# Optimization experiments

Measured on AMD Instinct MI355X. Metric: run time of the kernel, lower is better.

Reference implementation:

```python
import jax, jax.numpy as jnp
import numpy as np

HEADS = 16


def setup_inputs() -> dict:
    key = jax.random.key(0)
    k1, k2, k3, k4 = jax.random.split(key, 4)
    B, S, D = 2, 2048, 1024
    x = jax.random.normal(k1, (B, S, D), dtype=jnp.float32)
    scale = 0.02
    Wq = jax.random.normal(k2, (D, D), dtype=jnp.float32) * scale
    Wk = jax.random.normal(k3, (D, D), dtype=jnp.float32) * scale
    Wv = jax.random.normal(k4, (D, D), dtype=jnp.float32) * scale
    return {"x": x, "Wq": Wq, "Wk": Wk, "Wv": Wv}


def reference(x, Wq, Wk, Wv):
    B, S, D = x.shape
    H = HEADS
    dh = D // H
    # project and split heads: (B, S, D) -> (B, H, S, dh)
    def split_heads(t):
        return t.reshape(B, S, H, dh).transpose(0, 2, 1, 3)

    q = split_heads(x @ Wq)
    k = split_heads(x @ Wk)
    v = split_heads(x @ Wv)

    # scores: (B, H, S, S)
    scores = jnp.einsum("bhqd,bhkd->bhqk", q, k)
    causal_mask = jnp.triu(jnp.ones((S, S), dtype=bool), k=1)  # True above diagonal -> masked
    scores = jnp.where(causal_mask, -jnp.inf, scores) / jnp.sqrt(jnp.float32(dh))
    weights = jax.nn.softmax(scores, axis=-1)
    # dropout is identity at inference (eval mode)
    ctx = jnp.einsum("bhqk,bhkd->bhqd", weights, v)  # (B, H, S, dh)
    return ctx.transpose(0, 2, 1, 3).reshape(B, S, D)
```

## Files before the change

kernel.cpp:

```cpp
#include <hip/hip_runtime.h>
#include <hip/hip_bf16.h>
#include <cstdint>

#define BATCH  2
#define SEQ    2048
#define DMODEL 1024
#define NH     16
#define DH     64

typedef short bf16x8 __attribute__((ext_vector_type(8)));
typedef float f32x4  __attribute__((ext_vector_type(4)));
typedef unsigned short u16;

#define MFMA16(a, b, c) __builtin_amdgcn_mfma_f32_16x16x32_bf16((a), (b), (c), 0, 0, 0)

#define GLL(gp, lp) __builtin_amdgcn_global_load_lds( \
    (const __attribute__((address_space(1))) void*)(gp), \
    (__attribute__((address_space(3))) void*)(lp), 16, 0, 0)

#define SCL 0.18033688011112042f

#if __has_builtin(__builtin_amdgcn_exp2f)
#define EXP2(x) __builtin_amdgcn_exp2f(x)
#else
#define EXP2(x) __expf((x) * 0.69314718055994531f)
#endif

static __device__ __forceinline__ u16 f2bf(float f) {
  union { float f; unsigned int i; } u; u.f = f;
  unsigned int r = u.i + 0x7FFFu + ((u.i >> 16) & 1u);
  return (u16)(r >> 16);
}

__global__ __launch_bounds__(256) void convert_x_kernel(const float* __restrict__ X,
                                                        u16* __restrict__ Xb) {
  int idx = (blockIdx.x * 256 + threadIdx.x) * 8;
  float4 a = *reinterpret_cast<const float4*>(X + idx);
  float4 b = *reinterpret_cast<const float4*>(X + idx + 4);
  union { bf16x8 v; u16 u[8]; } pk;
  pk.u[0]=f2bf(a.x); pk.u[1]=f2bf(a.y); pk.u[2]=f2bf(a.z); pk.u[3]=f2bf(a.w);
  pk.u[4]=f2bf(b.x); pk.u[5]=f2bf(b.y); pk.u[6]=f2bf(b.z); pk.u[7]=f2bf(b.w);
  *reinterpret_cast<bf16x8*>(Xb + idx) = pk.v;
}

__global__ __launch_bounds__(256) void transpose_w_kernel(const float* __restrict__ W0,
                                                          const float* __restrict__ W1,
                                                          const float* __restrict__ W2,
                                                          u16* __restrict__ Wt) {
  const float* W = (blockIdx.z == 0) ? W0 : (blockIdx.z == 1) ? W1 : W2;
  const float sc = (blockIdx.z == 0) ? SCL : 1.0f;
  u16* out = Wt + (size_t)blockIdx.z * DMODEL * DMODEL;
  __shared__ float T[32][33];
  const int t = threadIdx.x;
  const int k0 = blockIdx.x * 32, n0 = blockIdx.y * 32;
  {
    int r = t >> 3, c = (t & 7) * 4;
    float4 v = *reinterpret_cast<const float4*>(W + (size_t)(k0 + r) * DMODEL + n0 + c);
    T[r][c] = v.x; T[r][c+1] = v.y; T[r][c+2] = v.z; T[r][c+3] = v.w;
  }
  __syncthreads();
  {
    int n = t >> 3, k = (t & 7) * 4;
    union { unsigned long long ll; u16 u[4]; } pk;
    pk.u[0] = f2bf(T[k][n] * sc);   pk.u[1] = f2bf(T[k+1][n] * sc);
    pk.u[2] = f2bf(T[k+2][n] * sc); pk.u[3] = f2bf(T[k+3][n] * sc);
    *reinterpret_cast<unsigned long long*>(out + (size_t)(n0 + n) * DMODEL + k0 + k) = pk.ll;
  }
}

__global__ __launch_bounds__(256) void qkv_mfma_kernel(const u16* __restrict__ Xb,
                                                       const u16* __restrict__ Wt,
                                                       u16* __restrict__ Y) {
  __shared__ u16 As[128 * 64];
  __shared__ u16 Bs[128 * 64];
  char* Ab = (char*)As; char* Bb = (char*)Bs;
  const int t = threadIdx.x;
  const int lane = t & 63;
  const int w = t >> 6;
  const int wr = w >> 1, wc = w & 1;
  const int l15 = lane & 15, lg = lane >> 4;
  const int row0 = blockIdx.x * 128;
  const int col0 = blockIdx.y * 128;
  const int z = blockIdx.z;
  const u16* Wz = Wt + (size_t)z * DMODEL * DMODEL;
  u16* Yz = Y + (size_t)z * ((size_t)BATCH * SEQ * DMODEL);

  f32x4 acc[4][4];
  #pragma unroll
  for (int mt = 0; mt < 4; ++mt)
    #pragma unroll
    for (int nt = 0; nt < 4; ++nt)
      acc[mt][nt] = (f32x4){0.f, 0.f, 0.f, 0.f};

  size_t aofs[4], bofs[4];
  #pragma unroll
  for (int it = 0; it < 4; ++it) {
    int row = it * 32 + (t >> 3);
    int sl  = (t & 7) ^ (row & 7);
    aofs[it] = (size_t)(row0 + row) * DMODEL + sl * 8;
    bofs[it] = (size_t)(col0 + row) * DMODEL + sl * 8;
  }

  for (int k0 = 0; k0 < DMODEL; k0 += 64) {
    __syncthreads();
    #pragma unroll
    for (int it = 0; it < 4; ++it) {
      GLL(Xb + aofs[it] + k0, Ab + it * 4096 + w * 1024);
      GLL(Wz + bofs[it] + k0, Bb + it * 4096 + w * 1024);
    }
    __syncthreads();
    #pragma unroll
    for (int c = 0; c < 2; ++c) {
      bf16x8 am[4], bn[4];
      int kof = c * 64 + lg * 16;
      #pragma unroll
      for (int mt = 0; mt < 4; ++mt) {
        int row = wr * 64 + mt * 16 + l15;
        am[mt] = *reinterpret_cast<const bf16x8*>(Ab + row * 128 + (kof ^ ((row & 7) << 4)));
      }
      #pragma unroll
      for (int nt = 0; nt < 4; ++nt) {
        int row = wc * 64 + nt * 16 + l15;
        bn[nt] = *reinterpret_cast<const bf16x8*>(Bb + row * 128 + (kof ^ ((row & 7) << 4)));
      }
      #pragma unroll
      for (int mt = 0; mt < 4; ++mt)
        #pragma unroll
        for (int nt = 0; nt < 4; ++nt)
          acc[mt][nt] = MFMA16(am[mt], bn[nt], acc[mt][nt]);
    }
  }

  #pragma unroll
  for (int mt = 0; mt < 4; ++mt) {
    #pragma unroll
    for (int i = 0; i < 4; ++i) {
      int bs = row0 + wr * 64 + mt * 16 + lg * 4 + i;
      int b = bs >> 11, s = bs & (SEQ - 1);
      #pragma unroll
      for (int nt = 0; nt < 4; ++nt) {
        int d = col0 + wc * 64 + nt * 16 + l15;
        int h = d >> 6, dd = d & (DH - 1);
        size_t off = (((size_t)b * NH + h) * SEQ + s) * DH + dd;
        Yz[off] = f2bf(acc[mt][nt][i]);
      }
    }
  }
}

__global__ __launch_bounds__(256) void transpose_v_kernel(const u16* __restrict__ V,
                                                          u16* __restrict__ Vt) {
  __shared__ u16 L[64][72];
  const int sb = blockIdx.x, h = blockIdx.y, b = blockIdx.z;
  const size_t hin  = ((size_t)b * NH + h) * (size_t)SEQ * DH;
  const size_t hout = ((size_t)b * NH + h) * (size_t)DH * SEQ;
  const int s0 = sb * 64;
  const int t = threadIdx.x;
  const int r = t >> 3, c = t & 7;
  #pragma unroll
  for (int it = 0; it < 2; ++it) {
    int row = r + it * 32;
    bf16x8 v = *reinterpret_cast<const bf16x8*>(V + hin + (size_t)(s0 + row) * DH + c * 8);
    *reinterpret_cast<bf16x8*>(&L[row][c * 8]) = v;
  }
  __syncthreads();
  #pragma unroll
  for (int it = 0; it < 2; ++it) {
    int d = r + it * 32;
    union { bf16x8 v; u16 u[8]; } pk;
    #pragma unroll
    for (int j = 0; j < 8; ++j) pk.u[j] = L[c * 8 + j][d];
    *reinterpret_cast<bf16x8*>(Vt + hout + (size_t)d * SEQ + s0 + c * 8) = pk.v;
  }
}

#define STAGE(kb)                                                     \
  {                                                                   \
    const u16* kp_ = Kw + hq + (size_t)(kb) * (64 * DH);              \
    const u16* vp_ = Vt + hv + (size_t)(kb) * 64;                     \
    _Pragma("unroll")                                                 \
    for (int it = 0; it < 8; ++it) {                                  \
      GLL(kp_ + kofs[it], (char*)Ksb + it * 1024);                    \
      GLL(vp_ + vofs[it], (char*)Vsb + it * 1024);                    \
    }                                                                 \
  }

#define WAITV()                                                       \
  asm volatile("s_waitcnt vmcnt(0)" ::: "memory");                    \
  __builtin_amdgcn_sched_barrier(0)

#define TILE(kbv, MASKED)                                                            \
  {                                                                                  \
    char* Kb = (char*)Ksb;                                                           \
    char* Vb = (char*)Vsb;                                                           \
    const int k0_ = (kbv) * 64;                                                      \
    __builtin_amdgcn_s_setprio(1);                                                   \
    _Pragma("unroll")                                                                \
    for (int kt = 0; kt < 4; ++kt) {                                                 \
      bf16x8 kf0 = *reinterpret_cast<const bf16x8*>(Kb + kvb0 + kt * 2048);          \
      bf16x8 kf1 = *reinterpret_cast<const bf16x8*>(Kb + kvb1 + kt * 2048);          \
      f32x4 sA = (f32x4){0.f, 0.f, 0.f, 0.f};                                        \
      f32x4 sB = (f32x4){0.f, 0.f, 0.f, 0.f};                                        \
      sA = MFMA16(kf0, qfA0, sA); sA = MFMA16(kf1, qfA1, sA);                        \
      sB = MFMA16(kf0, qfB0, sB); sB = MFMA16(kf1, qfB1, sB);                        \
      union { unsigned long long ll; __hip_bfloat16 bf[4]; } pA, pB;                 \
      _Pragma("unroll")                                                              \
      for (int i = 0; i < 4; ++i) {                                                  \
        float svA = sA[i], svB = sB[i];                                              \
        if (MASKED) {                                                                \
          int key = k0_ + kt * 16 + lg * 4 + i;                                      \
          if (key > qrowA) svA = -1e30f;                                             \
          if (key > qrowB) svB = -1e30f;                                             \
        }                                                                            \
        float eA = EXP2(svA), eB = EXP2(svB);                                        \
        l_A += eA; l_B += eB;                                                        \
        pA.bf[i] = __float2bfloat16(eA);                                             \
        pB.bf[i] = __float2bfloat16(eB);                                             \
      }                                                                              \
      int kx = (kt * 32) ^ xw;                                                       \
      *reinterpret_cast<unsigned long long*>(PbW + pwA + kx) = pA.ll;                \
      *reinterpret_cast<unsigned long long*>(PbW + pwB + kx) = pB.ll;                \
    }                                                                                \
    _Pragma("unroll")                                                                \
    for (int kc = 0; kc < 2; ++kc) {                                                 \
      const int tg = kc * 64;                                                        \
      bf16x8 paA = *reinterpret_cast<const bf16x8*>(PbW + (kvb0 ^ tg));              \
      bf16x8 paB = *reinterpret_cast<const bf16x8*>(PbW + (kvb0 ^ tg) + 2048);       \
      _Pragma("unroll")                                                              \
      for (int dt = 0; dt < 4; ++dt) {                                               \
        bf16x8 vv = *reinterpret_cast<const bf16x8*>(Vb + (kvb0 ^ tg) + dt * 2048);  \
        oA[dt] = MFMA16(paA, vv, oA[dt]);                                            \
        oB[dt] = MFMA16(paB, vv, oB[dt]);                                            \
      }                                                                              \
    }                                                                                \
    __builtin_amdgcn_s_setprio(0);                                                   \
  }

__global__ __launch_bounds__(64) void flash_mfma10_kernel(const u16* __restrict__ Qw,
                                                          const u16* __restrict__ Kw,
                                                          const u16* __restrict__ Vt,
                                                          float* __restrict__ Out) {
  __shared__ u16 Ksb[64 * 64];
  __shared__ u16 Vsb[64 * 64];
  __shared__ u16 Pw[32 * 64];

  const int wgid = blockIdx.x;
  const int g = wgid & 31;
  const int j = (wgid >> 5) & 7;
  const int r = wgid >> 8;
  const int qt = r * 8 + ((r & 1) ? (7 - j) : j);
  const int b = g >> 4, h = g & 15;
  const int nkv = (qt >> 1) + 1;

  const int lane = threadIdx.x;
  const int l15 = lane & 15, lg = lane >> 4;
  char* PbW = (char*)Pw;
  const size_t hq = ((size_t)b * NH + h) * (size_t)SEQ * DH;
  const size_t hv = ((size_t)b * NH + h) * (size_t)DH * SEQ;

  int kofs[8], vofs[8];
  #pragma unroll
  for (int it = 0; it < 8; ++it) {
    int idx = it * 64 + lane;
    int row = idx >> 3, sl = idx & 7;
    kofs[it] = row * DH  + ((sl ^ (row & 7)) * 8);
    vofs[it] = row * SEQ + ((sl ^ (row & 7)) * 8);
  }

  const int kvb0 = l15 * 128 + ((lg * 16) ^ ((l15 & 3) << 4)) + ((l15 & 4) << 4);
  const int kvb1 = kvb0 ^ 64;
  const int pwA  = l15 * 128 + ((lg * 8) ^ ((l15 & 1) << 4));
  const int pwB  = pwA + 2048;
  const int xw   = ((l15 >> 1) & 3) << 5;

  const int qbase = qt * 32;
  const int qrowA = qbase + l15;
  const int qrowB = qbase + 16 + l15;

  bf16x8 qfA0, qfA1, qfB0, qfB1;
  {
    const u16* qpA = Qw + hq + (size_t)qrowA * DH + lg * 8;
    const u16* qpB = Qw + hq + (size_t)qrowB * DH + lg * 8;
    qfA0 = *reinterpret_cast<const bf16x8*>(qpA);
    qfA1 = *reinterpret_cast<const bf16x8*>(qpA + 32);
    qfB0 = *reinterpret_cast<const bf16x8*>(qpB);
    qfB1 = *reinterpret_cast<const bf16x8*>(qpB + 32);
  }

  f32x4 oA[4], oB[4];
  #pragma unroll
  for (int dt = 0; dt < 4; ++dt) {
    oA[dt] = (f32x4){0.f, 0.f, 0.f, 0.f};
    oB[dt] = (f32x4){0.f, 0.f, 0.f, 0.f};
  }
  float l_A = 0.f, l_B = 0.f;

  #pragma unroll 1
  for (int kb = 0; kb < nkv - 1; ++kb) {
    STAGE(kb);
    WAITV();
    TILE(kb, 0);
  }
  STAGE(nkv - 1);
  WAITV();
  TILE(nkv - 1, 1);

  l_A += __shfl_xor(l_A, 16); l_A += __shfl_xor(l_A, 32);
  l_B += __shfl_xor(l_B, 16); l_B += __shfl_xor(l_B, 32);
  #pragma unroll
  for (int i = 0; i < 4; ++i) {
    float liA = __shfl(l_A, (lane & 48) + lg * 4 + i);
    float liB = __shfl(l_B, (lane & 48) + lg * 4 + i);
    float invA = 1.f / liA, invB = 1.f / liB;
    int qA = qbase + lg * 4 + i;
    int qB = qbase + 16 + lg * 4 + i;
    float* opA = Out + ((size_t)b * SEQ + qA) * DMODEL + h * DH + l15;
    float* opB = Out + ((size_t)b * SEQ + qB) * DMODEL + h * DH + l15;
    #pragma unroll
    for (int dt = 0; dt < 4; ++dt) {
      opA[dt * 16] = oA[dt][i] * invA;
      opB[dt * 16] = oB[dt][i] * invB;
    }
  }
}

extern "C" void kernel_launch(void* const* d_in, const int* in_sizes, int n_in,
                              void* d_out, int out_size, void* d_ws, size_t ws_size,
                              hipStream_t stream) {
  const float* x  = (const float*)d_in[0];
  const float* Wq = (const float*)d_in[1];
  const float* Wk = (const float*)d_in[2];
  const float* Wv = (const float*)d_in[3];
  float* out = (float*)d_out;

  u16* ws  = (u16*)d_ws;
  u16* qkv = ws;
  u16* xb  = ws + 12582912;
  u16* wt  = ws + 16777216;
  u16* vt  = ws + 19922944;

  convert_x_kernel<<<2048, 256, 0, stream>>>(x, xb);
  transpose_w_kernel<<<dim3(32, 32, 3), 256, 0, stream>>>(Wq, Wk, Wv, wt);
  qkv_mfma_kernel<<<dim3(32, 8, 3), 256, 0, stream>>>(xb, wt, qkv);
  transpose_v_kernel<<<dim3(32, NH, BATCH), 256, 0, stream>>>(qkv + 8388608, vt);
  flash_mfma10_kernel<<<2048, 64, 0, stream>>>(qkv, qkv + 4194304, vt, out);
}
```

Baseline: 99.11 us.

## Double-buffer K/V tiles in flash kernel and schedule longest query tiles first

Adds a second LDS buffer for K and V so the next tile's global-to-LDS loads are issued before computing the current tile. Partial vmcnt waits let those loads overlap the MFMA work. Workgroups are also reordered so the query tiles with the most KV blocks launch first, which is meant to reduce tail imbalance under the causal mask. LDS per single-wave workgroup grows from about 20KB to 36KB, which may reduce how many workgroups fit on a CU.

After: 93.35 us. 5.8% less time.

```diff
diff --git a/kernel.cpp b/kernel.cpp
--- a/kernel.cpp
+++ b/kernel.cpp
@@ -174,25 +174,25 @@
   }
 }
 
-#define STAGE(kb)                                                     \
+#define STAGE(KD, VD, kb)                                             \
   {                                                                   \
     const u16* kp_ = Kw + hq + (size_t)(kb) * (64 * DH);              \
     const u16* vp_ = Vt + hv + (size_t)(kb) * 64;                     \
     _Pragma("unroll")                                                 \
     for (int it = 0; it < 8; ++it) {                                  \
-      GLL(kp_ + kofs[it], (char*)Ksb + it * 1024);                    \
-      GLL(vp_ + vofs[it], (char*)Vsb + it * 1024);                    \
+      GLL(kp_ + kofs[it], (char*)(KD) + it * 1024);                   \
+      GLL(vp_ + vofs[it], (char*)(VD) + it * 1024);                   \
     }                                                                 \
   }
 
-#define WAITV()                                                       \
-  asm volatile("s_waitcnt vmcnt(0)" ::: "memory");                    \
+#define WAITC(N)                                                      \
+  asm volatile("s_waitcnt vmcnt(" #N ")" ::: "memory");               \
   __builtin_amdgcn_sched_barrier(0)
 
-#define TILE(kbv, MASKED)                                                            \
+#define TILE(kbv, KBUF, VBUF, MASKED)                                                \
   {                                                                                  \
-    char* Kb = (char*)Ksb;                                                           \
-    char* Vb = (char*)Vsb;                                                           \
+    char* Kb = (char*)(KBUF);                                                        \
+    char* Vb = (char*)(VBUF);                                                        \
     const int k0_ = (kbv) * 64;                                                      \
     __builtin_amdgcn_s_setprio(1);                                                   \
     _Pragma("unroll")                                                                \
@@ -236,19 +236,19 @@
     __builtin_amdgcn_s_setprio(0);                                                   \
   }
 
-__global__ __launch_bounds__(64) void flash_mfma10_kernel(const u16* __restrict__ Qw,
+__global__ __launch_bounds__(64) void flash_mfma11_kernel(const u16* __restrict__ Qw,
                                                           const u16* __restrict__ Kw,
                                                           const u16* __restrict__ Vt,
                                                           float* __restrict__ Out) {
-  __shared__ u16 Ksb[64 * 64];
-  __shared__ u16 Vsb[64 * 64];
+  __shared__ u16 KsA[64 * 64];
+  __shared__ u16 KsB[64 * 64];
+  __shared__ u16 VsA[64 * 64];
+  __shared__ u16 VsB[64 * 64];
   __shared__ u16 Pw[32 * 64];
 
   const int wgid = blockIdx.x;
   const int g = wgid & 31;
-  const int j = (wgid >> 5) & 7;
-  const int r = wgid >> 8;
-  const int qt = r * 8 + ((r & 1) ? (7 - j) : j);
+  const int qt = 63 - (wgid >> 5);
   const int b = g >> 4, h = g & 15;
   const int nkv = (qt >> 1) + 1;
 
@@ -295,15 +295,28 @@
   }
   float l_A = 0.f, l_B = 0.f;
 
+  STAGE(KsA, VsA, 0);
+  int kb = 0;
   #pragma unroll 1
-  for (int kb = 0; kb < nkv - 1; ++kb) {
-    STAGE(kb);
-    WAITV();
-    TILE(kb, 0);
-  }
-  STAGE(nkv - 1);
-  WAITV();
-  TILE(nkv - 1, 1);
+  while (kb + 2 < nkv) {
+    STAGE(KsB, VsB, kb + 1);
+    WAITC(16);
+    TILE(kb, KsA, VsA, 0);
+    STAGE(KsA, VsA, kb + 2);
+    WAITC(16);
+    TILE(kb + 1, KsB, VsB, 0);
+    kb += 2;
+  }
+  if (kb + 2 == nkv) {
+    STAGE(KsB, VsB, kb + 1);
+    WAITC(16);
+    TILE(kb, KsA, VsA, 0);
+    WAITC(0);
+    TILE(kb + 1, KsB, VsB, 1);
+  } else {
+    WAITC(0);
+    TILE(kb, KsA, VsA, 1);
+  }
 
   l_A += __shfl_xor(l_A, 16); l_A += __shfl_xor(l_A, 32);
   l_B += __shfl_xor(l_B, 16); l_B += __shfl_xor(l_B, 32);
@@ -343,5 +356,5 @@
   transpose_w_kernel<<<dim3(32, 32, 3), 256, 0, stream>>>(Wq, Wk, Wv, wt);
   qkv_mfma_kernel<<<dim3(32, 8, 3), 256, 0, stream>>>(xb, wt, qkv);
   transpose_v_kernel<<<dim3(32, NH, BATCH), 256, 0, stream>>>(qkv + 8388608, vt);
-  flash_mfma10_kernel<<<2048, 64, 0, stream>>>(qkv, qkv + 4194304, vt, out);
-}
+  flash_mfma11_kernel<<<2048, 64, 0, stream>>>(qkv, qkv + 4194304, vt, out);
+}
```

## Split long causal rows across two workgroups and read K/V directly from global

Applied to the files above, without the earlier changes.

Query tiles in the upper half are split into two KV-range partitions, each written as an unnormalized bf16 partial with row sums, and a new reduce kernel combines them. The aim is to balance causal work across workgroups and shorten the tail, using 3072 workgroups instead of 2048. The LDS staging of K and V through global_load_lds is also removed, so MFMA operands are read straight from global memory. This cuts LDS use and barriers but depends on cache hits, and it adds an extra launch plus bf16 rounding of the partial outputs. Combining without a max is valid because the kernel never subtracts a running max.

Result: slower. 126.8 us (+27.9%).

```diff
diff --git a/kernel.cpp b/kernel.cpp
--- a/kernel.cpp
+++ b/kernel.cpp
@@ -30,6 +30,11 @@
   union { float f; unsigned int i; } u; u.f = f;
   unsigned int r = u.i + 0x7FFFu + ((u.i >> 16) & 1u);
   return (u16)(r >> 16);
+}
+
+static __device__ __forceinline__ float bf2f(u16 v) {
+  union { unsigned int i; float f; } u; u.i = ((unsigned int)v) << 16;
+  return u.f;
 }
 
 __global__ __launch_bounds__(256) void convert_x_kernel(const float* __restrict__ X,
@@ -174,83 +179,73 @@
   }
 }
 
-#define STAGE(kb)                                                     \
-  {                                                                   \
-    const u16* kp_ = Kw + hq + (size_t)(kb) * (64 * DH);              \
-    const u16* vp_ = Vt + hv + (size_t)(kb) * 64;                     \
-    _Pragma("unroll")                                                 \
-    for (int it = 0; it < 8; ++it) {                                  \
-      GLL(kp_ + kofs[it], (char*)Ksb + it * 1024);                    \
-      GLL(vp_ + vofs[it], (char*)Vsb + it * 1024);                    \
-    }                                                                 \
-  }
-
-#define WAITV()                                                       \
-  asm volatile("s_waitcnt vmcnt(0)" ::: "memory");                    \
-  __builtin_amdgcn_sched_barrier(0)
-
-#define TILE(kbv, MASKED)                                                            \
-  {                                                                                  \
-    char* Kb = (char*)Ksb;                                                           \
-    char* Vb = (char*)Vsb;                                                           \
-    const int k0_ = (kbv) * 64;                                                      \
-    __builtin_amdgcn_s_setprio(1);                                                   \
-    _Pragma("unroll")                                                                \
-    for (int kt = 0; kt < 4; ++kt) {                                                 \
-      bf16x8 kf0 = *reinterpret_cast<const bf16x8*>(Kb + kvb0 + kt * 2048);          \
-      bf16x8 kf1 = *reinterpret_cast<const bf16x8*>(Kb + kvb1 + kt * 2048);          \
-      f32x4 sA = (f32x4){0.f, 0.f, 0.f, 0.f};                                        \
-      f32x4 sB = (f32x4){0.f, 0.f, 0.f, 0.f};                                        \
-      sA = MFMA16(kf0, qfA0, sA); sA = MFMA16(kf1, qfA1, sA);                        \
-      sB = MFMA16(kf0, qfB0, sB); sB = MFMA16(kf1, qfB1, sB);                        \
-      union { unsigned long long ll; __hip_bfloat16 bf[4]; } pA, pB;                 \
-      _Pragma("unroll")                                                              \
-      for (int i = 0; i < 4; ++i) {                                                  \
-        float svA = sA[i], svB = sB[i];                                              \
-        if (MASKED) {                                                                \
-          int key = k0_ + kt * 16 + lg * 4 + i;                                      \
-          if (key > qrowA) svA = -1e30f;                                             \
-          if (key > qrowB) svB = -1e30f;                                             \
-        }                                                                            \
-        float eA = EXP2(svA), eB = EXP2(svB);                                        \
-        l_A += eA; l_B += eB;                                                        \
-        pA.bf[i] = __float2bfloat16(eA);                                             \
-        pB.bf[i] = __float2bfloat16(eB);                                             \
-      }                                                                              \
-      int kx = (kt * 32) ^ xw;                                                       \
-      *reinterpret_cast<unsigned long long*>(PbW + pwA + kx) = pA.ll;                \
-      *reinterpret_cast<unsigned long long*>(PbW + pwB + kx) = pB.ll;                \
-    }                                                                                \
-    _Pragma("unroll")                                                                \
-    for (int kc = 0; kc < 2; ++kc) {                                                 \
-      const int tg = kc * 64;                                                        \
-      bf16x8 paA = *reinterpret_cast<const bf16x8*>(PbW + (kvb0 ^ tg));              \
-      bf16x8 paB = *reinterpret_cast<const bf16x8*>(PbW + (kvb0 ^ tg) + 2048);       \
-      _Pragma("unroll")                                                              \
-      for (int dt = 0; dt < 4; ++dt) {                                               \
-        bf16x8 vv = *reinterpret_cast<const bf16x8*>(Vb + (kvb0 ^ tg) + dt * 2048);  \
-        oA[dt] = MFMA16(paA, vv, oA[dt]);                                            \
-        oB[dt] = MFMA16(paB, vv, oB[dt]);                                            \
-      }                                                                              \
-    }                                                                                \
-    __builtin_amdgcn_s_setprio(0);                                                   \
-  }
-
-__global__ __launch_bounds__(64) void flash_mfma10_kernel(const u16* __restrict__ Qw,
-                                                          const u16* __restrict__ Kw,
-                                                          const u16* __restrict__ Vt,
-                                                          float* __restrict__ Out) {
-  __shared__ u16 Ksb[64 * 64];
-  __shared__ u16 Vsb[64 * 64];
+#define TILE(kbv, MASKED)                                                             \
+  {                                                                                   \
+    const int k0_ = (kbv) * 64;                                                       \
+    const u16* kp_ = Kw + hq + (size_t)k0_ * DH;                                      \
+    const u16* vp_ = Vt + hv + k0_;                                                   \
+    __builtin_amdgcn_s_setprio(1);                                                    \
+    _Pragma("unroll")                                                                 \
+    for (int kt = 0; kt < 4; ++kt) {                                                  \
+      const u16* kr_ = kp_ + (kt * 16 + l15) * DH + lg * 8;                           \
+      bf16x8 kf0 = *reinterpret_cast<const bf16x8*>(kr_);                             \
+      bf16x8 kf1 = *reinterpret_cast<const bf16x8*>(kr_ + 32);                        \
+      f32x4 sA = (f32x4){0.f, 0.f, 0.f, 0.f};                                         \
+      f32x4 sB = (f32x4){0.f, 0.f, 0.f, 0.f};                                         \
+      sA = MFMA16(kf0, qfA0, sA); sA = MFMA16(kf1, qfA1, sA);                         \
+      sB = MFMA16(kf0, qfB0, sB); sB = MFMA16(kf1, qfB1, sB);                         \
+      union { unsigned long long ll; __hip_bfloat16 bf[4]; } pA, pB;                  \
+      _Pragma("unroll")                                                               \
+      for (int i = 0; i < 4; ++i) {                                                   \
+        float svA = sA[i], svB = sB[i];                                               \
+        if (MASKED) {                                                                 \
+          int key = k0_ + kt * 16 + lg * 4 + i;                                       \
+          if (key > qrowA) svA = -1e30f;                                              \
+          if (key > qrowB) svB = -1e30f;                                              \
+        }                                                                             \
+        float eA = EXP2(svA), eB = EXP2(svB);                                         \
+        l_A += eA; l_B += eB;                                                         \
+        pA.bf[i] = __float2bfloat16(eA);                                              \
+        pB.bf[i] = __float2bfloat16(eB);                                              \
+      }                                                                               \
+      int kx = (kt * 32) ^ xw;                                                        \
+      *reinterpret_cast<unsigned long long*>(PbW + pwA + kx) = pA.ll;                 \
+      *reinterpret_cast<unsigned long long*>(PbW + pwB + kx) = pB.ll;                 \
+    }                                                                                 \
+    _Pragma("unroll")                                                                 \
+    for (int kc = 0; kc < 2; ++kc) {                                                  \
+      const int tg = kc * 64;                                                         \
+      bf16x8 paA = *reinterpret_cast<const bf16x8*>(PbW + (kvb0 ^ tg));               \
+      bf16x8 paB = *reinterpret_cast<const bf16x8*>(PbW + (kvb0 ^ tg) + 2048);        \
+      _Pragma("unroll")                                                               \
+      for (int dt = 0; dt < 4; ++dt) {                                                \
+        bf16x8 vv = *reinterpret_cast<const bf16x8*>(vp_ + (size_t)(dt * 16 + l15) * SEQ + kc * 32 + lg * 8); \
+        oA[dt] = MFMA16(paA, vv, oA[dt]);                                             \
+        oB[dt] = MFMA16(paB, vv, oB[dt]);                                             \
+      }                                                                               \
+    }                                                                                 \
+    __builtin_amdgcn_s_setprio(0);                                                    \
+  }
+
+__global__ __launch_bounds__(64) void flash_part_kernel(const u16* __restrict__ Qw,
+                                                        const u16* __restrict__ Kw,
+                                                        const u16* __restrict__ Vt,
+                                                        u16* __restrict__ Pws,
+                                                        float* __restrict__ Out) {
   __shared__ u16 Pw[32 * 64];
 
   const int wgid = blockIdx.x;
+  const int up = wgid >> 5;
   const int g = wgid & 31;
-  const int j = (wgid >> 5) & 7;
-  const int r = wgid >> 8;
-  const int qt = r * 8 + ((r & 1) ? (7 - j) : j);
+  int qt, c;
+  if (up < 32)      { qt = 32 + up;   c = 0; }
+  else if (up < 64) { qt = 63 - up;   c = 0; }
+  else              { qt = 127 - up;  c = 1; }
   const int b = g >> 4, h = g & 15;
   const int nkv = (qt >> 1) + 1;
+  const int kbeg = c * 16;
+  const int kend = (qt >= 32 && c == 0) ? 16 : nkv;
+  const bool hasdiag = (kend == nkv);
 
   const int lane = threadIdx.x;
   const int l15 = lane & 15, lg = lane >> 4;
@@ -258,17 +253,7 @@
   const size_t hq = ((size_t)b * NH + h) * (size_t)SEQ * DH;
   const size_t hv = ((size_t)b * NH + h) * (size_t)DH * SEQ;
 
-  int kofs[8], vofs[8];
-  #pragma unroll
-  for (int it = 0; it < 8; ++it) {
-    int idx = it * 64 + lane;
-    int row = idx >> 3, sl = idx & 7;
-    kofs[it] = row * DH  + ((sl ^ (row & 7)) * 8);
-    vofs[it] = row * SEQ + ((sl ^ (row & 7)) * 8);
-  }
-
   const int kvb0 = l15 * 128 + ((lg * 16) ^ ((l15 & 3) << 4)) + ((l15 & 4) << 4);
-  const int kvb1 = kvb0 ^ 64;
   const int pwA  = l15 * 128 + ((lg * 8) ^ ((l15 & 1) << 4));
   const int pwB  = pwA + 2048;
   const int xw   = ((l15 >> 1) & 3) << 5;
@@ -296,31 +281,62 @@
   float l_A = 0.f, l_B = 0.f;
 
   #pragma unroll 1
-  for (int kb = 0; kb < nkv - 1; ++kb) {
-    STAGE(kb);
-    WAITV();
+  for (int kb = kbeg; kb < kend - 1; ++kb) {
     TILE(kb, 0);
   }
-  STAGE(nkv - 1);
-  WAITV();
-  TILE(nkv - 1, 1);
+  if (hasdiag) { TILE(kend - 1, 1); } else { TILE(kend - 1, 0); }
 
   l_A += __shfl_xor(l_A, 16); l_A += __shfl_xor(l_A, 32);
   l_B += __shfl_xor(l_B, 16); l_B += __shfl_xor(l_B, 32);
-  #pragma unroll
-  for (int i = 0; i < 4; ++i) {
-    float liA = __shfl(l_A, (lane & 48) + lg * 4 + i);
-    float liB = __shfl(l_B, (lane & 48) + lg * 4 + i);
-    float invA = 1.f / liA, invB = 1.f / liB;
-    int qA = qbase + lg * 4 + i;
-    int qB = qbase + 16 + lg * 4 + i;
-    float* opA = Out + ((size_t)b * SEQ + qA) * DMODEL + h * DH + l15;
-    float* opB = Out + ((size_t)b * SEQ + qB) * DMODEL + h * DH + l15;
-    #pragma unroll
-    for (int dt = 0; dt < 4; ++dt) {
-      opA[dt * 16] = oA[dt][i] * invA;
-      opB[dt * 16] = oB[dt][i] * invB;
-    }
+
+  if (qt < 32) {
+    #pragma unroll
+    for (int i = 0; i < 4; ++i) {
+      float liA = __shfl(l_A, (lane & 48) + lg * 4 + i);
+      float liB = __shfl(l_B, (lane & 48) + lg * 4 + i);
+      float invA = 1.f / liA, invB = 1.f / liB;
+      int qA = qbase + lg * 4 + i;
+      int qB = qbase + 16 + lg * 4 + i;
+      float* opA = Out + ((size_t)b * SEQ + qA) * DMODEL + h * DH + l15;
+      float* opB = Out + ((size_t)b * SEQ + qB) * DMODEL + h * DH + l15;
+      #pragma unroll
+      for (int dt = 0; dt < 4; ++dt) {
+        opA[dt * 16] = oA[dt][i] * invA;
+        opB[dt * 16] = oB[dt][i] * invB;
+      }
+    }
+  } else {
+    const int u2 = (qt - 32) * 2 + c;
+    u16* po = Pws + (size_t)(u2 * 32 + g) * 2112;
+    float* pl = (float*)(po + 2048);
+    if (lg == 0) pl[l15] = l_A;
+    if (lg == 1) pl[16 + l15] = l_B;
+    #pragma unroll
+    for (int i = 0; i < 4; ++i) {
+      #pragma unroll
+      for (int dt = 0; dt < 4; ++dt) {
+        po[(lg * 4 + i) * 64 + dt * 16 + l15]      = f2bf(oA[dt][i]);
+        po[(16 + lg * 4 + i) * 64 + dt * 16 + l15] = f2bf(oB[dt][i]);
+      }
+    }
+  }
+}
+
+__global__ __launch_bounds__(64) void flash_reduce_kernel(const u16* __restrict__ Pws,
+                                                          float* __restrict__ Out) {
+  const int qt = 32 + blockIdx.x;
+  const int g = blockIdx.y;
+  const int b = g >> 4, h = g & 15;
+  const int lane = threadIdx.x;
+  const u16* p0 = Pws + (size_t)(((qt - 32) * 2 + 0) * 32 + g) * 2112;
+  const u16* p1 = Pws + (size_t)(((qt - 32) * 2 + 1) * 32 + g) * 2112;
+  const float* l0 = (const float*)(p0 + 2048);
+  const float* l1 = (const float*)(p1 + 2048);
+  #pragma unroll 4
+  for (int q = 0; q < 32; ++q) {
+    float inv = 1.f / (l0[q] + l1[q]);
+    float o = bf2f(p0[q * 64 + lane]) + bf2f(p1[q * 64 + lane]);
+    Out[((size_t)b * SEQ + qt * 32 + q) * DMODEL + h * DH + lane] = o * inv;
   }
 }
 
@@ -338,10 +354,12 @@
   u16* xb  = ws + 12582912;
   u16* wt  = ws + 16777216;
   u16* vt  = ws + 19922944;
+  u16* pp  = xb;
 
   convert_x_kernel<<<2048, 256, 0, stream>>>(x, xb);
   transpose_w_kernel<<<dim3(32, 32, 3), 256, 0, stream>>>(Wq, Wk, Wv, wt);
   qkv_mfma_kernel<<<dim3(32, 8, 3), 256, 0, stream>>>(xb, wt, qkv);
   transpose_v_kernel<<<dim3(32, NH, BATCH), 256, 0, stream>>>(qkv + 8388608, vt);
-  flash_mfma10_kernel<<<2048, 64, 0, stream>>>(qkv, qkv + 4194304, vt, out);
-}
+  flash_part_kernel<<<3072, 64, 0, stream>>>(qkv, qkv + 4194304, vt, pp, out);
+  flash_reduce_kernel<<<dim3(32, 32), 64, 0, stream>>>(pp, out);
+}
```
